# Kernel optimization log

Hardware: AMD Instinct MI355X
Metric: run time of the kernel (lower is better)

The kernel has to match this reference:

```python
import jax, jax.numpy as jnp
import numpy as np

B, T, C, H = 2, 2048, 2048, 16
D = C // H  # head size = 128
ROPE_BASE = 10000.0


def setup_inputs() -> dict:
    key = jax.random.key(0)
    k1, k2, k3 = jax.random.split(key, 3)
    scale = 1.0 / np.sqrt(C)
    x = jax.random.normal(k1, (B, T, C), dtype=jnp.float32)
    w_qkv = jax.random.normal(k2, (3 * C, C), dtype=jnp.float32) * scale
    w_o = jax.random.normal(k3, (C, C), dtype=jnp.float32) * scale
    # rope cache: complex exp(i * pos * theta_j), stored as cos/sin, shape [T, D//2]
    inv_freq = 1.0 / (ROPE_BASE ** (np.arange(0, D, 2, dtype=np.float32) / D))  # [D//2]
    angles = np.arange(T, dtype=np.float32)[:, None] * inv_freq[None, :]        # [T, D//2]
    rope_cos = jnp.asarray(np.cos(angles))
    rope_sin = jnp.asarray(np.sin(angles))
    return {"x": x, "w_qkv": w_qkv, "w_o": w_o, "rope_cos": rope_cos, "rope_sin": rope_sin}


def _apply_rope(x, cos, sin):
    # x: [B, T, H, D]; cos/sin: [T, D//2]
    xr = x.reshape(*x.shape[:-1], D // 2, 2)
    x0, x1 = xr[..., 0], xr[..., 1]
    c = cos[None, :, None, :]
    s = sin[None, :, None, :]
    # complex multiply (x0 + i x1) * (c + i s)
    out = jnp.stack([x0 * c - x1 * s, x0 * s + x1 * c], axis=-1)
    return out.reshape(x.shape)


def reference(x, w_qkv, w_o, rope_cos, rope_sin):
    Bs, Ts, Cs = x.shape
    qkv = jnp.einsum('btc,ec->bte', x, w_qkv)  # [B, T, 3C]
    q, k, v = jnp.split(qkv, 3, axis=-1)
    q = q.reshape(Bs, Ts, H, D)
    k = k.reshape(Bs, Ts, H, D)
    v = v.reshape(Bs, Ts, H, D)
    q = _apply_rope(q, rope_cos[:Ts], rope_sin[:Ts])
    k = _apply_rope(k, rope_cos[:Ts], rope_sin[:Ts])
    scores = jnp.einsum('bthd,bshd->bhts', q, k) / jnp.sqrt(jnp.float32(D))
    causal = jnp.tril(jnp.ones((Ts, Ts), dtype=bool))
    scores = jnp.where(causal[None, None], scores, jnp.finfo(scores.dtype).min)
    attn = jax.nn.softmax(scores, axis=-1)
    y = jnp.einsum('bhts,bshd->bthd', attn, v).reshape(Bs, Ts, Cs)
    return jnp.einsum('btc,oc->bto', y, w_o)
```

## Files before the change

### kernel.cpp

```cpp
#include <hip/hip_runtime.h>
#include <cstdint>
#include <cstddef>

#define DEVI __device__ __forceinline__

typedef __attribute__((ext_vector_type(8))) short short8;
typedef __attribute__((ext_vector_type(4))) float f32x4;
typedef __attribute__((ext_vector_type(16))) float f32x16;
typedef __attribute__((ext_vector_type(4))) unsigned int u32x4;

static constexpr int Bdim = 2, T = 2048, C = 2048, H = 16, D = 128;
static constexpr int CQ = 3 * C;

DEVI unsigned short f2bf(float f) {
  unsigned int u = __float_as_uint(f);
  u = (u + 0x7fffu + ((u >> 16) & 1u)) >> 16;
  return (unsigned short)u;
}
DEVI float bf2f(unsigned int u) { return __uint_as_float(u << 16); }

DEVI unsigned int cvtpk(float lo, float hi) {
  unsigned int r;
  asm("v_cvt_pk_bf16_f32 %0, %1, %2" : "=v"(r) : "v"(lo), "v"(hi));
  return r;
}

DEVI void gload_lds16(const void* g, void* l) {
  __builtin_amdgcn_global_load_lds((const __attribute__((address_space(1))) void*)g,
                                   (__attribute__((address_space(3))) void*)l, 16, 0, 0);
}

__global__ __launch_bounds__(256) void convert_bf16(const float* __restrict__ src,
                                                    unsigned short* __restrict__ dst, int n) {
  const int i = (blockIdx.x * 256 + threadIdx.x) * 4;
  if (i >= n) return;
  float4 v = *(const float4*)&src[i];
  uint2 o;
  o.x = (unsigned)f2bf(v.x) | ((unsigned)f2bf(v.y) << 16);
  o.y = (unsigned)f2bf(v.z) | ((unsigned)f2bf(v.w) << 16);
  *(uint2*)&dst[i] = o;
}

template <int OUT_BF16>
__global__ __launch_bounds__(256) void gemm_bt(const unsigned short* __restrict__ A,
                                               const unsigned short* __restrict__ Bm,
                                               void* __restrict__ outp,
                                               int M, int N, int Kd) {
  __shared__ __align__(16) unsigned short lds_a[128 * 64];
  __shared__ __align__(16) unsigned short lds_b[128 * 64];
  const int tid = threadIdx.x;
  const int wid = tid >> 6, lane = tid & 63;
  const int lg = lane >> 4, lc = lane & 15;
  const int m0 = blockIdx.y * 128, n0 = blockIdx.x * 128;
  const int wr = (wid >> 1) * 64, wc = (wid & 1) * 64;
  const int srow = wid * 8 + (lane >> 3);
  const int schunk = lane & 7;

  f32x4 acc[4][4] = {};

  for (int k0 = 0; k0 < Kd; k0 += 64) {
    __syncthreads();
#pragma unroll
    for (int j = 0; j < 4; ++j) {
      const int row = j * 32 + srow;
      const int cc = schunk ^ (row & 7);
      gload_lds16(&A[(size_t)(m0 + row) * Kd + k0 + cc * 8], &lds_a[j * 2048 + wid * 512]);
      gload_lds16(&Bm[(size_t)(n0 + row) * Kd + k0 + cc * 8], &lds_b[j * 2048 + wid * 512]);
    }
    __syncthreads();
    __builtin_amdgcn_s_setprio(1);
#pragma unroll
    for (int kk = 0; kk < 2; ++kk) {
      short8 af[4], bf[4];
#pragma unroll
      for (int m = 0; m < 4; ++m) {
        const int row = wr + m * 16 + lc;
        af[m] = *(const short8*)&lds_a[row * 64 + (((kk * 4 + lg) ^ (row & 7)) * 8)];
      }
#pragma unroll
      for (int n = 0; n < 4; ++n) {
        const int row = wc + n * 16 + lc;
        bf[n] = *(const short8*)&lds_b[row * 64 + (((kk * 4 + lg) ^ (row & 7)) * 8)];
      }
#pragma unroll
      for (int m = 0; m < 4; ++m)
#pragma unroll
        for (int n = 0; n < 4; ++n)
          acc[m][n] = __builtin_amdgcn_mfma_f32_16x16x32_bf16(af[m], bf[n], acc[m][n], 0, 0, 0);
    }
    __builtin_amdgcn_s_setprio(0);
  }

#pragma unroll
  for (int m = 0; m < 4; ++m)
#pragma unroll
    for (int n = 0; n < 4; ++n)
#pragma unroll
      for (int r = 0; r < 4; ++r) {
        const int row = m0 + wr + m * 16 + lg * 4 + r;
        const int col = n0 + wc + n * 16 + lc;
        const float v = acc[m][n][r];
        if (OUT_BF16)
          ((unsigned short*)outp)[(size_t)row * N + col] = f2bf(v);
        else
          ((float*)outp)[(size_t)row * N + col] = v;
      }
}

__global__ __launch_bounds__(256) void rope_kernel(const unsigned short* __restrict__ qkv,
                                                   const float* __restrict__ cosb,
                                                   const float* __restrict__ sinb,
                                                   unsigned short* __restrict__ Qr,
                                                   unsigned short* __restrict__ Kr) {
  const int idx = blockIdx.x * 256 + threadIdx.x;
  const int i = idx & 63;
  const int h = (idx >> 6) & (H - 1);
  const int tg = idx >> 10;
  const int t = tg & (T - 1);
  const int b = tg >> 11;
  const float c = cosb[t * 64 + i], s = sinb[t * 64 + i];
  const unsigned short* row = qkv + (size_t)tg * CQ;
  const unsigned int q = *(const unsigned int*)&row[h * D + 2 * i];
  const unsigned int k = *(const unsigned int*)&row[C + h * D + 2 * i];
  const float q0 = bf2f(q & 0xffffu), q1 = bf2f(q >> 16);
  const float k0 = bf2f(k & 0xffffu), k1 = bf2f(k >> 16);
  const float SC = 0.08838834764831845f * 1.4426950408889634f;
  const float q0r = (q0 * c - q1 * s) * SC, q1r = (q0 * s + q1 * c) * SC;
  const float k0r = k0 * c - k1 * s, k1r = k0 * s + k1 * c;
  const size_t off = ((size_t)(b * H + h) * T + t) * D + 2 * i;
  *(unsigned int*)&Qr[off] = (unsigned)f2bf(q0r) | ((unsigned)f2bf(q1r) << 16);
  *(unsigned int*)&Kr[off] = (unsigned)f2bf(k0r) | ((unsigned)f2bf(k1r) << 16);
}

__global__ __launch_bounds__(256) void transpose_v(const unsigned short* __restrict__ qkv,
                                                   unsigned short* __restrict__ Vt) {
  __shared__ unsigned short tile[64][65];
  const int bh = blockIdx.z, b = bh >> 4, h = bh & (H - 1);
  const int t0 = blockIdx.x * 64, d0 = blockIdx.y * 64;
  const int tx = threadIdx.x & 63, ty = threadIdx.x >> 6;
#pragma unroll
  for (int rr = 0; rr < 64; rr += 4)
    tile[rr + ty][tx] = qkv[(size_t)(b * T + t0 + rr + ty) * CQ + 2 * C + h * D + d0 + tx];
  __syncthreads();
#pragma unroll
  for (int rr = 0; rr < 64; rr += 4)
    Vt[((size_t)bh * D + d0 + rr + ty) * T + t0 + tx] = tile[tx][rr + ty];
}

__global__ __launch_bounds__(256, 2) void flash_attn(const unsigned short* __restrict__ Q,
                                                     const unsigned short* __restrict__ K,
                                                     const unsigned short* __restrict__ Vt,
                                                     unsigned short* __restrict__ Y) {
  __shared__ __align__(16) unsigned short ldsK[64 * 128];
  __shared__ __align__(16) unsigned short ldsV[64 * 128];

  const int bid = blockIdx.x;
  const int lid = (bid & 7) * 64 + (bid >> 3);
  const int bh = lid >> 4;
  const int qt = 15 - (lid & 15);
  const int wid = threadIdx.x >> 6;
  const int lane = threadIdx.x & 63;
  const int l31 = lane & 31, l15 = lane & 15;
  const int hi = lane >> 5;
  const int b = bh >> 4, h = bh & (H - 1);
  const int q0w = qt * 128 + wid * 32;
  const int qrow = q0w + l31;

  const unsigned short* Qh = Q + (size_t)bh * T * D;
  const unsigned short* Kh = K + (size_t)bh * T * D;
  const unsigned short* Vh = Vt + (size_t)bh * D * T;

  const int sr = lane >> 4;

  short8 qf[8];
#pragma unroll
  for (int ds = 0; ds < 8; ++ds)
    qf[ds] = *(const short8*)&Qh[(size_t)qrow * D + ds * 16 + hi * 8];

  f32x16 oacc[4] = {};
  float m_run = -1e30f, l_run = 0.f;

  u32x4 rK[4], rV[4];

#pragma unroll
  for (int j = 0; j < 4; ++j) {
    const int r0 = (wid * 4 + j) * 4;
    const int row = r0 + sr;
    const int cc = l15 ^ (row & 15);
    rK[j] = *(const u32x4*)&Kh[(size_t)row * D + cc * 8];
    const int cv = l15 ^ (row & 15);
    const int d = row + ((cv >> 3) << 6);
    rV[j] = *(const u32x4*)&Vh[(size_t)d * T + (cv & 7) * 8];
  }

  const int ntb = 2 * qt + 2;
  for (int t = 0; t < ntb; ++t) {
    const int kv0 = t * 64;

    __builtin_amdgcn_s_barrier();

#pragma unroll
    for (int j = 0; j < 4; ++j) {
      const int r0 = (wid * 4 + j) * 4;
      *(u32x4*)((char*)ldsK + r0 * 256 + lane * 16) = rK[j];
      *(u32x4*)((char*)ldsV + r0 * 256 + lane * 16) = rV[j];
    }
    asm volatile("s_waitcnt lgkmcnt(0)" ::: "memory");
    __builtin_amdgcn_s_barrier();
    __builtin_amdgcn_sched_barrier(0);

    if (t + 1 < ntb) {
      const int kvn = kv0 + 64;
#pragma unroll
      for (int j = 0; j < 4; ++j) {
        const int r0 = (wid * 4 + j) * 4;
        const int row = r0 + sr;
        const int cc = l15 ^ (row & 15);
        rK[j] = *(const u32x4*)&Kh[(size_t)(kvn + row) * D + cc * 8];
        const int d = row + ((cc >> 3) << 6);
        rV[j] = *(const u32x4*)&Vh[(size_t)d * T + kvn + (cc & 7) * 8];
      }
    }
    __builtin_amdgcn_sched_barrier(0);

    if (kv0 <= q0w + 31) {
      f32x16 s0 = {}, s1 = {};
      __builtin_amdgcn_s_setprio(1);
#pragma unroll
      for (int ds = 0; ds < 8; ++ds) {
        const int cs = ((ds * 2 + hi) ^ l15) * 8;
        const short8 k0 = *(const short8*)&ldsK[l31 * 128 + cs];
        const short8 k1 = *(const short8*)&ldsK[(32 + l31) * 128 + cs];
        s0 = __builtin_amdgcn_mfma_f32_32x32x16_bf16(k0, qf[ds], s0, 0, 0, 0);
        s1 = __builtin_amdgcn_mfma_f32_32x32x16_bf16(k1, qf[ds], s1, 0, 0, 0);
      }
      __builtin_amdgcn_s_setprio(0);

      if (kv0 + 63 > q0w) {
#pragma unroll
        for (int r = 0; r < 16; ++r) {
          const int kvr = kv0 + (r & 3) + 8 * (r >> 2) + 4 * hi;
          s0[r] = (kvr <= qrow) ? s0[r] : -1e30f;
          s1[r] = (kvr + 32 <= qrow) ? s1[r] : -1e30f;
        }
      }

      float mt[8];
#pragma unroll
      for (int r = 0; r < 8; ++r)
        mt[r] = fmaxf(fmaxf(s0[r], s0[r + 8]), fmaxf(s1[r], s1[r + 8]));
#pragma unroll
      for (int r = 0; r < 4; ++r) mt[r] = fmaxf(mt[r], mt[r + 4]);
      float mx = fmaxf(fmaxf(mt[0], mt[1]), fmaxf(mt[2], mt[3]));
      mx = fmaxf(mx, __shfl_xor(mx, 32));
      const float mnew = fmaxf(m_run, mx);
      if (__any(mnew > m_run)) {
        const float f = exp2f(m_run - mnew);
        m_run = mnew;
        l_run *= f;
#pragma unroll
        for (int blk = 0; blk < 4; ++blk) oacc[blk] *= f;
      }
#pragma unroll
      for (int r = 0; r < 16; ++r) {
        s0[r] = exp2f(s0[r] - m_run);
        s1[r] = exp2f(s1[r] - m_run);
      }
      {
        float a0 = 0.f, a1 = 0.f, a2 = 0.f, a3 = 0.f;
#pragma unroll
        for (int r = 0; r < 16; r += 4) {
          a0 += s0[r] + s1[r];
          a1 += s0[r + 1] + s1[r + 1];
          a2 += s0[r + 2] + s1[r + 2];
          a3 += s0[r + 3] + s1[r + 3];
        }
        l_run += (a0 + a1) + (a2 + a3);
      }

      __builtin_amdgcn_s_setprio(1);
#pragma unroll
      for (int ks = 0; ks < 4; ++ks) {
        const int rb = (ks & 1) * 8;
        const f32x16& S = (ks < 2) ? s0 : s1;
        const unsigned int w0 = cvtpk(S[rb + 0], S[rb + 1]);
        const unsigned int w1 = cvtpk(S[rb + 2], S[rb + 3]);
        const unsigned int w2 = cvtpk(S[rb + 4], S[rb + 5]);
        const unsigned int w3 = cvtpk(S[rb + 6], S[rb + 7]);
        const unsigned int x0 = (unsigned int)__shfl_xor((int)w0, 32);
        const unsigned int x1 = (unsigned int)__shfl_xor((int)w1, 32);
        const unsigned int x2 = (unsigned int)__shfl_xor((int)w2, 32);
        const unsigned int x3 = (unsigned int)__shfl_xor((int)w3, 32);
        u32x4 av;
        av[0] = hi ? x2 : w0;
        av[1] = hi ? x3 : w1;
        av[2] = hi ? w2 : x0;
        av[3] = hi ? w3 : x1;
        const short8 pf = __builtin_bit_cast(short8, av);
#pragma unroll
        for (int blk = 0; blk < 4; ++blk) {
          const int row2 = (blk & 1) * 32 + l31;
          const int cs = ((((blk >> 1) * 8) + ks * 2 + hi) ^ l15) * 8;
          const short8 vf = *(const short8*)&ldsV[row2 * 128 + cs];
          oacc[blk] = __builtin_amdgcn_mfma_f32_32x32x16_bf16(vf, pf, oacc[blk], 0, 0, 0);
        }
      }
      __builtin_amdgcn_s_setprio(0);
    }
  }

  const float l = l_run + __shfl_xor(l_run, 32);
  const float inv = 1.0f / l;
  unsigned short* yrow = Y + ((size_t)(b * T + qrow)) * C + h * D;
#pragma unroll
  for (int blk = 0; blk < 4; ++blk)
#pragma unroll
    for (int g = 0; g < 4; ++g) {
      const int d0 = blk * 32 + 8 * g + 4 * hi;
      uint2 st;
      st.x = cvtpk(oacc[blk][4 * g + 0] * inv, oacc[blk][4 * g + 1] * inv);
      st.y = cvtpk(oacc[blk][4 * g + 2] * inv, oacc[blk][4 * g + 3] * inv);
      *(uint2*)&yrow[d0] = st;
    }
}

extern "C" void kernel_launch(void* const* d_in, const int* in_sizes, int n_in,
                              void* d_out, int out_size, void* d_ws, size_t ws_size,
                              hipStream_t stream) {
  const float* x = (const float*)d_in[0];
  const float* wqkv = (const float*)d_in[1];
  const float* wo = (const float*)d_in[2];
  const float* rc = (const float*)d_in[3];
  const float* rs = (const float*)d_in[4];
  float* out = (float*)d_out;
  char* ws = (char*)d_ws;

  unsigned short* xb    = (unsigned short*)(ws + 0);
  unsigned short* wqkvb = (unsigned short*)(ws + 16777216);
  unsigned short* qkv   = (unsigned short*)(ws + 41943040);
  unsigned short* Qr    = (unsigned short*)(ws + 92274688);
  unsigned short* Kr    = (unsigned short*)(ws + 109051904);
  unsigned short* Vt  = xb;
  unsigned short* Yb  = qkv;
  unsigned short* wob = wqkvb;

  convert_bf16<<<8192, 256, 0, stream>>>(x, xb, Bdim * T * C);
  convert_bf16<<<12288, 256, 0, stream>>>(wqkv, wqkvb, CQ * C);
  gemm_bt<1><<<dim3(CQ / 128, (Bdim * T) / 128), 256, 0, stream>>>(xb, wqkvb, (void*)qkv,
                                                                   Bdim * T, CQ, C);
  rope_kernel<<<(Bdim * T * H * 64) / 256, 256, 0, stream>>>(qkv, rc, rs, Qr, Kr);
  transpose_v<<<dim3(T / 64, D / 64, Bdim * H), 256, 0, stream>>>(qkv, Vt);
  convert_bf16<<<4096, 256, 0, stream>>>(wo, wob, C * C);
  flash_attn<<<512, 256, 0, stream>>>(Qr, Kr, Vt, Yb);
  gemm_bt<0><<<dim3(C / 128, (Bdim * T) / 128), 256, 0, stream>>>(Yb, wob, (void*)out,
                                                                  Bdim * T, C, C);
}
```

Measured before the change: 272.8 us.

## Double-buffer GEMM LDS tiles and switch to 32x32x16 MFMA

Splits the GEMM shared-memory tiles into two buffers so the next K-slice's global-to-LDS loads are issued before the MFMA work on the current slice, leaving one barrier per iteration instead of two. It also replaces the 16x16x32 MFMA tiling with 32x32x16 instructions, so each wave does fewer LDS fragment reads per MFMA. LDS use doubles to 64KB per block, which may lower occupancy. The last iteration prefetches a wasted tile from k=0.

New measurement: 293.2 us. +7.5%, slower.

```diff
diff --git a/kernel.cpp b/kernel.cpp
--- a/kernel.cpp
+++ b/kernel.cpp
@@ -46,65 +46,84 @@
                                                const unsigned short* __restrict__ Bm,
                                                void* __restrict__ outp,
                                                int M, int N, int Kd) {
-  __shared__ __align__(16) unsigned short lds_a[128 * 64];
-  __shared__ __align__(16) unsigned short lds_b[128 * 64];
+  __shared__ __align__(16) unsigned short lds_a[2][128 * 64];
+  __shared__ __align__(16) unsigned short lds_b[2][128 * 64];
   const int tid = threadIdx.x;
   const int wid = tid >> 6, lane = tid & 63;
-  const int lg = lane >> 4, lc = lane & 15;
+  const int l31 = lane & 31;
+  const int hi = lane >> 5;
   const int m0 = blockIdx.y * 128, n0 = blockIdx.x * 128;
   const int wr = (wid >> 1) * 64, wc = (wid & 1) * 64;
   const int srow = wid * 8 + (lane >> 3);
   const int schunk = lane & 7;
 
-  f32x4 acc[4][4] = {};
-
+  f32x16 acc[2][2] = {};
+
+#pragma unroll
+  for (int j = 0; j < 4; ++j) {
+    const int row = j * 32 + srow;
+    const int cc = schunk ^ (row & 7);
+    gload_lds16(&A[(size_t)(m0 + row) * Kd + cc * 8], &lds_a[0][j * 2048 + wid * 512]);
+    gload_lds16(&Bm[(size_t)(n0 + row) * Kd + cc * 8], &lds_b[0][j * 2048 + wid * 512]);
+  }
+
+  int cur = 0;
   for (int k0 = 0; k0 < Kd; k0 += 64) {
-    __syncthreads();
+    asm volatile("s_waitcnt vmcnt(0)" ::: "memory");
+    __builtin_amdgcn_s_barrier();
+    __builtin_amdgcn_sched_barrier(0);
+
+    const int kn = (k0 + 64 < Kd) ? k0 + 64 : 0;
 #pragma unroll
     for (int j = 0; j < 4; ++j) {
       const int row = j * 32 + srow;
       const int cc = schunk ^ (row & 7);
-      gload_lds16(&A[(size_t)(m0 + row) * Kd + k0 + cc * 8], &lds_a[j * 2048 + wid * 512]);
-      gload_lds16(&Bm[(size_t)(n0 + row) * Kd + k0 + cc * 8], &lds_b[j * 2048 + wid * 512]);
-    }
-    __syncthreads();
+      gload_lds16(&A[(size_t)(m0 + row) * Kd + kn + cc * 8],
+                  &lds_a[cur ^ 1][j * 2048 + wid * 512]);
+      gload_lds16(&Bm[(size_t)(n0 + row) * Kd + kn + cc * 8],
+                  &lds_b[cur ^ 1][j * 2048 + wid * 512]);
+    }
+    __builtin_amdgcn_sched_barrier(0);
+
     __builtin_amdgcn_s_setprio(1);
 #pragma unroll
-    for (int kk = 0; kk < 2; ++kk) {
-      short8 af[4], bf[4];
-#pragma unroll
-      for (int m = 0; m < 4; ++m) {
-        const int row = wr + m * 16 + lc;
-        af[m] = *(const short8*)&lds_a[row * 64 + (((kk * 4 + lg) ^ (row & 7)) * 8)];
-      }
-#pragma unroll
-      for (int n = 0; n < 4; ++n) {
-        const int row = wc + n * 16 + lc;
-        bf[n] = *(const short8*)&lds_b[row * 64 + (((kk * 4 + lg) ^ (row & 7)) * 8)];
-      }
-#pragma unroll
-      for (int m = 0; m < 4; ++m)
-#pragma unroll
-        for (int n = 0; n < 4; ++n)
-          acc[m][n] = __builtin_amdgcn_mfma_f32_16x16x32_bf16(af[m], bf[n], acc[m][n], 0, 0, 0);
+    for (int kk = 0; kk < 4; ++kk) {
+      short8 af[2], bf[2];
+#pragma unroll
+      for (int m = 0; m < 2; ++m) {
+        const int row = wr + m * 32 + l31;
+        af[m] = *(const short8*)&lds_a[cur][row * 64 + (((kk * 2 + hi) ^ (row & 7)) * 8)];
+      }
+#pragma unroll
+      for (int n = 0; n < 2; ++n) {
+        const int row = wc + n * 32 + l31;
+        bf[n] = *(const short8*)&lds_b[cur][row * 64 + (((kk * 2 + hi) ^ (row & 7)) * 8)];
+      }
+#pragma unroll
+      for (int m = 0; m < 2; ++m)
+#pragma unroll
+        for (int n = 0; n < 2; ++n)
+          acc[m][n] = __builtin_amdgcn_mfma_f32_32x32x16_bf16(af[m], bf[n], acc[m][n], 0, 0, 0);
     }
     __builtin_amdgcn_s_setprio(0);
+    cur ^= 1;
   }
 
 #pragma unroll
-  for (int m = 0; m < 4; ++m)
-#pragma unroll
-    for (int n = 0; n < 4; ++n)
-#pragma unroll
-      for (int r = 0; r < 4; ++r) {
-        const int row = m0 + wr + m * 16 + lg * 4 + r;
-        const int col = n0 + wc + n * 16 + lc;
+  for (int m = 0; m < 2; ++m)
+#pragma unroll
+    for (int n = 0; n < 2; ++n) {
+      const int col = n0 + wc + n * 32 + l31;
+#pragma unroll
+      for (int r = 0; r < 16; ++r) {
+        const int row = m0 + wr + m * 32 + (r & 3) + 8 * (r >> 2) + 4 * hi;
         const float v = acc[m][n][r];
         if (OUT_BF16)
           ((unsigned short*)outp)[(size_t)row * N + col] = f2bf(v);
         else
           ((float*)outp)[(size_t)row * N + col] = v;
       }
+    }
 }
 
 __global__ __launch_bounds__(256) void rope_kernel(const unsigned short* __restrict__ qkv,
```

## Fuse RoPE, Q scaling and V transpose into the QKV GEMM epilogue

Applied to the files above, without the earlier changes.

The QKV projection GEMM now writes rotated and scaled Q, rotated K, and transposed V directly from its accumulators, using a lane shuffle to pair adjacent dimensions for the rotary multiply. This removes the separate rope and transpose kernels and the round trip of the intermediate bf16 qkv buffer through global memory. In exchange the epilogue does scattered 2-byte stores for Q/K with a T*D stride and per-element cos/sin loads, which may coalesce poorly.

After: 290.4 us. 6.5% more time.

```diff
diff --git a/kernel.cpp b/kernel.cpp
--- a/kernel.cpp
+++ b/kernel.cpp
@@ -41,11 +41,16 @@
   *(uint2*)&dst[i] = o;
 }
 
-template <int OUT_BF16>
+template <int MODE>
 __global__ __launch_bounds__(256) void gemm_bt(const unsigned short* __restrict__ A,
                                                const unsigned short* __restrict__ Bm,
                                                void* __restrict__ outp,
-                                               int M, int N, int Kd) {
+                                               int M, int N, int Kd,
+                                               unsigned short* __restrict__ Qr,
+                                               unsigned short* __restrict__ Kr,
+                                               unsigned short* __restrict__ Vt,
+                                               const float* __restrict__ cosb,
+                                               const float* __restrict__ sinb) {
   __shared__ __align__(16) unsigned short lds_a[128 * 64];
   __shared__ __align__(16) unsigned short lds_b[128 * 64];
   const int tid = threadIdx.x;
@@ -91,60 +96,50 @@
     __builtin_amdgcn_s_setprio(0);
   }
 
-#pragma unroll
-  for (int m = 0; m < 4; ++m)
-#pragma unroll
-    for (int n = 0; n < 4; ++n)
-#pragma unroll
-      for (int r = 0; r < 4; ++r) {
-        const int row = m0 + wr + m * 16 + lg * 4 + r;
-        const int col = n0 + wc + n * 16 + lc;
-        const float v = acc[m][n][r];
-        if (OUT_BF16)
-          ((unsigned short*)outp)[(size_t)row * N + col] = f2bf(v);
-        else
-          ((float*)outp)[(size_t)row * N + col] = v;
-      }
-}
-
-__global__ __launch_bounds__(256) void rope_kernel(const unsigned short* __restrict__ qkv,
-                                                   const float* __restrict__ cosb,
-                                                   const float* __restrict__ sinb,
-                                                   unsigned short* __restrict__ Qr,
-                                                   unsigned short* __restrict__ Kr) {
-  const int idx = blockIdx.x * 256 + threadIdx.x;
-  const int i = idx & 63;
-  const int h = (idx >> 6) & (H - 1);
-  const int tg = idx >> 10;
-  const int t = tg & (T - 1);
-  const int b = tg >> 11;
-  const float c = cosb[t * 64 + i], s = sinb[t * 64 + i];
-  const unsigned short* row = qkv + (size_t)tg * CQ;
-  const unsigned int q = *(const unsigned int*)&row[h * D + 2 * i];
-  const unsigned int k = *(const unsigned int*)&row[C + h * D + 2 * i];
-  const float q0 = bf2f(q & 0xffffu), q1 = bf2f(q >> 16);
-  const float k0 = bf2f(k & 0xffffu), k1 = bf2f(k >> 16);
-  const float SC = 0.08838834764831845f * 1.4426950408889634f;
-  const float q0r = (q0 * c - q1 * s) * SC, q1r = (q0 * s + q1 * c) * SC;
-  const float k0r = k0 * c - k1 * s, k1r = k0 * s + k1 * c;
-  const size_t off = ((size_t)(b * H + h) * T + t) * D + 2 * i;
-  *(unsigned int*)&Qr[off] = (unsigned)f2bf(q0r) | ((unsigned)f2bf(q1r) << 16);
-  *(unsigned int*)&Kr[off] = (unsigned)f2bf(k0r) | ((unsigned)f2bf(k1r) << 16);
-}
-
-__global__ __launch_bounds__(256) void transpose_v(const unsigned short* __restrict__ qkv,
-                                                   unsigned short* __restrict__ Vt) {
-  __shared__ unsigned short tile[64][65];
-  const int bh = blockIdx.z, b = bh >> 4, h = bh & (H - 1);
-  const int t0 = blockIdx.x * 64, d0 = blockIdx.y * 64;
-  const int tx = threadIdx.x & 63, ty = threadIdx.x >> 6;
-#pragma unroll
-  for (int rr = 0; rr < 64; rr += 4)
-    tile[rr + ty][tx] = qkv[(size_t)(b * T + t0 + rr + ty) * CQ + 2 * C + h * D + d0 + tx];
-  __syncthreads();
-#pragma unroll
-  for (int rr = 0; rr < 64; rr += 4)
-    Vt[((size_t)bh * D + d0 + rr + ty) * T + t0 + tx] = tile[tx][rr + ty];
+  if (MODE == 0) {
+#pragma unroll
+    for (int m = 0; m < 4; ++m)
+#pragma unroll
+      for (int n = 0; n < 4; ++n)
+#pragma unroll
+        for (int r = 0; r < 4; ++r) {
+          const int row = m0 + wr + m * 16 + lg * 4 + r;
+          const int col = n0 + wc + n * 16 + lc;
+          ((float*)outp)[(size_t)row * N + col] = acc[m][n][r];
+        }
+  } else {
+    const int region = n0 >> 11;
+    const int h = (n0 & 2047) >> 7;
+    const float SCQ = 0.08838834764831845f * 1.4426950408889634f;
+#pragma unroll
+    for (int m = 0; m < 4; ++m)
+#pragma unroll
+      for (int n = 0; n < 4; ++n) {
+        const int d = wc + n * 16 + lc;
+        const int row0 = m0 + wr + m * 16 + lg * 4;
+        const int b = row0 >> 11;
+        const int t0 = row0 & (T - 1);
+        if (region < 2) {
+          unsigned short* dst = (region == 0 ? Qr : Kr) + ((size_t)(b * H + h) * T) * D + d;
+          const int i = d >> 1;
+#pragma unroll
+          for (int r = 0; r < 4; ++r) {
+            const int t = t0 + r;
+            const float v = acc[m][n][r];
+            const float p = __shfl_xor(v, 1);
+            const float c = cosb[t * 64 + i], s = sinb[t * 64 + i];
+            float o = (d & 1) ? (p * s + v * c) : (v * c - p * s);
+            if (region == 0) o *= SCQ;
+            dst[(size_t)t * D] = f2bf(o);
+          }
+        } else {
+          uint2 st;
+          st.x = cvtpk(acc[m][n][0], acc[m][n][1]);
+          st.y = cvtpk(acc[m][n][2], acc[m][n][3]);
+          *(uint2*)&Vt[((size_t)(b * H + h) * D + d) * T + t0] = st;
+        }
+      }
+  }
 }
 
 __global__ __launch_bounds__(256, 2) void flash_attn(const unsigned short* __restrict__ Q,
@@ -337,21 +332,18 @@
 
   unsigned short* xb    = (unsigned short*)(ws + 0);
   unsigned short* wqkvb = (unsigned short*)(ws + 16777216);
-  unsigned short* qkv   = (unsigned short*)(ws + 41943040);
+  unsigned short* Yb    = (unsigned short*)(ws + 41943040);
+  unsigned short* Vt    = (unsigned short*)(ws + 58720256);
   unsigned short* Qr    = (unsigned short*)(ws + 92274688);
   unsigned short* Kr    = (unsigned short*)(ws + 109051904);
-  unsigned short* Vt  = xb;
-  unsigned short* Yb  = qkv;
-  unsigned short* wob = wqkvb;
+  unsigned short* wob   = wqkvb;
 
   convert_bf16<<<8192, 256, 0, stream>>>(x, xb, Bdim * T * C);
   convert_bf16<<<12288, 256, 0, stream>>>(wqkv, wqkvb, CQ * C);
-  gemm_bt<1><<<dim3(CQ / 128, (Bdim * T) / 128), 256, 0, stream>>>(xb, wqkvb, (void*)qkv,
-                                                                   Bdim * T, CQ, C);
-  rope_kernel<<<(Bdim * T * H * 64) / 256, 256, 0, stream>>>(qkv, rc, rs, Qr, Kr);
-  transpose_v<<<dim3(T / 64, D / 64, Bdim * H), 256, 0, stream>>>(qkv, Vt);
+  gemm_bt<2><<<dim3(CQ / 128, (Bdim * T) / 128), 256, 0, stream>>>(
+      xb, wqkvb, nullptr, Bdim * T, CQ, C, Qr, Kr, Vt, rc, rs);
   convert_bf16<<<4096, 256, 0, stream>>>(wo, wob, C * C);
   flash_attn<<<512, 256, 0, stream>>>(Qr, Kr, Vt, Yb);
-  gemm_bt<0><<<dim3(C / 128, (Bdim * T) / 128), 256, 0, stream>>>(Yb, wob, (void*)out,
-                                                                  Bdim * T, C, C);
-}
+  gemm_bt<0><<<dim3(C / 128, (Bdim * T) / 128), 256, 0, stream>>>(
+      Yb, wob, (void*)out, Bdim * T, C, C, nullptr, nullptr, nullptr, nullptr, nullptr);
+}
```
